# Kernel tuning notes

Measured on AMD Instinct MI355X. Metric: run time of the kernel, lower is better.

Reference implementation:

```python
import jax, jax.numpy as jnp
import numpy as np

S, D = 16384, 1024


def setup_inputs() -> dict:
    key = jax.random.key(0)
    ks = jax.random.split(key, 7)
    stdv = 1.0 / np.sqrt(D)
    u = lambda k, shape: jax.random.uniform(k, shape, jnp.float32, -stdv, stdv)
    return {
        "x": jax.random.normal(ks[0], (S, D), jnp.float32),
        "Wq": u(ks[1], (D, D)), "bq": u(ks[2], (D,)),
        "Wk": u(ks[3], (D, D)), "bk": u(ks[4], (D,)),
        "Wv": u(ks[5], (D, D)), "bv": u(ks[6], (D,)),
    }


def reference(x, Wq, bq, Wk, bk, Wv, bv):
    # torch.nn.Linear: y = x @ W^T + b
    q = x @ Wq.T + bq          # [S, D]
    k = x @ Wk.T + bk          # [S, D]
    v = x @ Wv.T + bv          # [S, D]
    d = x.shape[-1]
    # NOTE: faithful to source -- scores are over the FEATURE axis: [D, D]
    scores = jnp.einsum('sd,se->de', q, k) / jnp.sqrt(jnp.float32(d))
    attn = jax.nn.softmax(scores, axis=-1)   # [D, D]
    out = v @ attn                           # [S, D]
    return out, attn
```

## Files before the change

kernel.cpp:

```cpp
#include <hip/hip_runtime.h>
#include <hip/hip_bf16.h>
#include <stdint.h>


#define S_ 16384
#define D_ 1024

typedef _Float16 half8 __attribute__((ext_vector_type(8)));
typedef _Float16 half4 __attribute__((ext_vector_type(4)));
typedef float f32x4 __attribute__((ext_vector_type(4)));

__device__ __forceinline__ void gload_lds16(const _Float16* g, _Float16* l) {
    __builtin_amdgcn_global_load_lds(
        (const __attribute__((address_space(1))) void*)g,
        (__attribute__((address_space(3))) void*)l, 16, 0, 0);
}

#define VM8() do { asm volatile("s_waitcnt vmcnt(8)" ::: "memory"); __builtin_amdgcn_sched_barrier(0); } while (0)
#define VM0() do { asm volatile("s_waitcnt vmcnt(0)" ::: "memory"); __builtin_amdgcn_sched_barrier(0); } while (0)
#define BAR() __builtin_amdgcn_s_barrier()
#define LGKM0() do { asm volatile("s_waitcnt lgkmcnt(0)" ::: "memory"); __builtin_amdgcn_sched_barrier(0); } while (0)
#define LGKM8() do { asm volatile("s_waitcnt lgkmcnt(8)" ::: "memory"); __builtin_amdgcn_sched_barrier(0); } while (0)
#define PRIO1() __builtin_amdgcn_s_setprio(1)
#define PRIO0() __builtin_amdgcn_s_setprio(0)

#define PAIR10(PI, BY, BX) do { \
    if ((PI) < 4) { BY = 0; BX = (PI); } \
    else if ((PI) < 7) { BY = 1; BX = (PI) - 3; } \
    else if ((PI) < 9) { BY = 2; BX = (PI) - 5; } \
    else { BY = 3; BX = 3; } \
} while (0)

#define STAGEA(H, KT, NX) do { \
    const _Float16* _s = srcA + (size_t)((H) * 128) * 16384 + (size_t)(KT) * 64; \
    _Float16* _d = AsS + (NX) * 16384 + ((H) * 128 + 8 * w) * 64; \
    gload_lds16(_s, _d); \
    gload_lds16(_s + (size_t)64 * 16384, _d + 4096); \
} while (0)

#define STAGEB(H, KT, NX) do { \
    const _Float16* _s = srcB + (size_t)((H) * 128) * 16384 + (size_t)(KT) * 64; \
    _Float16* _d = BsS + (NX) * 16384 + ((H) * 128 + 8 * w) * 64; \
    gload_lds16(_s, _d); \
    gload_lds16(_s + (size_t)64 * 16384, _d + 4096); \
} while (0)

#define READA(PA, QA) do { _Pragma("unroll") \
    for (int fm = 0; fm < 4; ++fm) { \
        af[fm][0] = *(const half8*)((PA) + (((QA) * 128 + fm * 16) << 7) + cx0); \
        af[fm][1] = *(const half8*)((PA) + (((QA) * 128 + fm * 16) << 7) + cx1); } \
} while (0)

#define READB(PB, BF, QB) do { _Pragma("unroll") \
    for (int fn = 0; fn < 2; ++fn) { \
        BF[fn][0] = *(const half8*)((PB) + (((QB) * 128 + fn * 16) << 7) + cx0); \
        BF[fn][1] = *(const half8*)((PB) + (((QB) * 128 + fn * 16) << 7) + cx1); } \
} while (0)

#define MFMAB(QA, QB, BF) do { _Pragma("unroll") \
    for (int fm = 0; fm < 4; ++fm) { _Pragma("unroll") \
        for (int fn = 0; fn < 2; ++fn) { \
            f32x4 _c = acc[(QA) * 4 + fm][(QB) * 2 + fn]; \
            _c = __builtin_amdgcn_mfma_f32_16x16x32_f16(af[fm][0], BF[fn][0], _c, 0, 0, 0); \
            _c = __builtin_amdgcn_mfma_f32_16x16x32_f16(af[fm][1], BF[fn][1], _c, 0, 0, 0); \
            acc[(QA) * 4 + fm][(QB) * 2 + fn] = _c; } } \
} while (0)

__global__ __launch_bounds__(512, 2)
void g_and_prep(const _Float16* __restrict__ A, _Float16* __restrict__ C,
                const float* __restrict__ Wq, const float* __restrict__ Wk,
                const float* __restrict__ Wv, const float* __restrict__ bq,
                const float* __restrict__ m,
                _Float16* __restrict__ wq16, _Float16* __restrict__ wk16,
                _Float16* __restrict__ wvT16,
                float* __restrict__ u2, float* __restrict__ wvec) {
    __shared__ _Float16 SM2[65536];
    const int t = threadIdx.x;

    if (blockIdx.x < 160) {
        _Float16* AsS = SM2;
        _Float16* BsS = SM2 + 32768;
        const int l = t & 63;
        const int w = t >> 6;
        const int wm = w >> 2, wn = w & 3;

        const int hb = blockIdx.x;
        const int lg = (hb & 7) * 20 + (hb >> 3);
        const int bz = lg / 10;
        const int pi = lg - bz * 10;
        int by, bx;
        PAIR10(pi, by, bx);
        const size_t m0 = (size_t)by * 256;
        const size_t n0 = (size_t)bx * 256;
        const size_t k0 = (size_t)bz * 1024;
        const long long coff = (long long)bz * 1048576LL;

        const int colsw = 8 * ((l & 7) ^ (l >> 3));
        const _Float16* srcA = A + (m0 + 8 * w + (l >> 3)) * (size_t)16384 + k0 + colsw;
        const _Float16* srcB = A + (n0 + 8 * w + (l >> 3)) * (size_t)16384 + k0 + colsw;

        const int cx0 = (((l >> 4) << 4)) ^ ((l & 7) << 4);
        const int cx1 = (64 + ((l >> 4) << 4)) ^ ((l & 7) << 4);
        const char* basePA = (const char*)AsS + ((wm * 64 + (l & 15)) << 7);
        const char* basePB = (const char*)BsS + ((wn * 32 + (l & 15)) << 7);

        f32x4 acc[8][4] = {};
        half8 af[4][2], bf0[2][2], bf1[2][2];

        const int nk = 16;

        STAGEA(0, 0, 0); STAGEB(0, 0, 0); STAGEB(1, 0, 0); STAGEA(1, 0, 0);
        STAGEA(0, 1, 1); STAGEB(0, 1, 1); STAGEB(1, 1, 1); STAGEA(1, 1, 1);

        for (int kt = 0; kt < nk; ++kt) {
            const int p = kt & 1;
            const int ks = kt + 2;
            const bool hs = ks < nk;
            const char* pA = basePA + p * 32768;
            const char* pB = basePB + p * 32768;

            if (kt == nk - 1) VM0(); else VM8();
            BAR();

            READA(pA, 0); READB(pB, bf0, 0);
            LGKM8();
            BAR(); LGKM0();
            PRIO1(); MFMAB(0, 0, bf0); PRIO0(); BAR();

            READB(pB, bf1, 1);
            if (hs) { STAGEA(0, ks, p); STAGEB(0, ks, p); }
            BAR(); LGKM0();
            PRIO1(); MFMAB(0, 1, bf1); PRIO0(); BAR();

            READA(pA, 1);
            if (hs) STAGEB(1, ks, p);
            BAR(); LGKM0();
            PRIO1(); MFMAB(1, 1, bf1); PRIO0(); BAR();

            if (hs) STAGEA(1, ks, p);
            PRIO1(); MFMAB(1, 0, bf0); PRIO0(); BAR();
        }

        _Float16* eb = SM2;
        const int cr = (l >> 4) << 2;
        const int cc = l & 15;
#pragma unroll
        for (int h = 0; h < 2; ++h) {
            BAR();
#pragma unroll
            for (int mm = 0; mm < 4; ++mm) {
#pragma unroll
                for (int n = 0; n < 4; ++n) {
                    const int lrow0 = wm * 64 + mm * 16 + cr;
                    const int lcol = (n >> 1) * 128 + wn * 32 + (n & 1) * 16 + cc;
#pragma unroll
                    for (int r = 0; r < 4; ++r)
                        eb[(lrow0 + r) * 264 + lcol] = (_Float16)acc[h * 4 + mm][n][r];
                }
            }
            LGKM0();
            BAR();
#pragma unroll
            for (int i = 0; i < 8; ++i) {
                const int lrow = w * 16 + i * 2 + (l >> 5);
                const half8 v = *(const half8*)(eb + lrow * 264 + (l & 31) * 8);
                const size_t row = m0 + (size_t)h * 128 + lrow;
                const size_t col = n0 + (l & 31) * 8;
                __builtin_nontemporal_store(v,
                    (half8*)(C + coff + (long long)row * 1024 + col));
            }
            LGKM0();
        }
        return;
    }

    const int h = t >> 8;
    const int vt = t & 255;
    const int vb = (blockIdx.x - 160) * 2 + h;
    _Float16* tileh = SM2 + h * 4224;
    float* wredAll = (float*)(SM2 + 16896);
    const bool isW = vb < 1024;

    if (isW) {
        const bool isQ = vb < 512;
        const int bb = isQ ? vb : vb - 512;
        const float* W = isQ ? Wq : Wk;
        _Float16* o = isQ ? wq16 : wk16;
        const size_t base = (size_t)bb * 2048 + (size_t)vt * 8;
        const f32x4* p = (const f32x4*)(W + base);
        f32x4 x0 = p[0], x1 = p[1];
        half8 hv;
        hv[0] = (_Float16)x0[0]; hv[1] = (_Float16)x0[1];
        hv[2] = (_Float16)x0[2]; hv[3] = (_Float16)x0[3];
        hv[4] = (_Float16)x1[0]; hv[5] = (_Float16)x1[1];
        hv[6] = (_Float16)x1[2]; hv[7] = (_Float16)x1[3];
        ((half8*)o)[bb * 256 + vt] = hv;
        const int col = (vt * 8) & 1023;
        f32x4 m0v = *(const f32x4*)(m + col);
        f32x4 m1v = *(const f32x4*)(m + col + 4);
        float s = x0[0] * m0v[0] + x0[1] * m0v[1] + x0[2] * m0v[2] + x0[3] * m0v[3]
                + x1[0] * m1v[0] + x1[1] * m1v[1] + x1[2] * m1v[2] + x1[3] * m1v[3];
        for (int o2 = 32; o2; o2 >>= 1) s += __shfl_xor(s, o2);
        if ((t & 63) == 0) wredAll[t >> 6] = s;
    } else {
        const int bb = vb - 1024;
        const int c0 = (bb & 15) * 64;
        const int r0 = (bb >> 4) * 64;
        const int cg = vt & 15;
        const int rb = vt >> 4;
#pragma unroll
        for (int it = 0; it < 4; ++it) {
            const int rr = rb + it * 16;
            f32x4 v = *(const f32x4*)(Wv + (size_t)(r0 + rr) * 1024 + c0 + cg * 4);
            tileh[rr * 66 + cg * 4 + 0] = (_Float16)v[0];
            tileh[rr * 66 + cg * 4 + 1] = (_Float16)v[1];
            tileh[rr * 66 + cg * 4 + 2] = (_Float16)v[2];
            tileh[rr * 66 + cg * 4 + 3] = (_Float16)v[3];
        }
    }
    __syncthreads();
    if (isW) {
        if (vt == 0) {
            const bool isQ = vb < 512;
            const int bb = isQ ? vb : vb - 512;
            const int rA = 2 * bb, rB = 2 * bb + 1;
            const float vA = wredAll[h * 4 + 0] + wredAll[h * 4 + 1];
            const float vB = wredAll[h * 4 + 2] + wredAll[h * 4 + 3];
            if (isQ) {
                u2[rA] = vA + 16384.0f * bq[rA];
                u2[rB] = vB + 16384.0f * bq[rB];
            } else {
                wvec[rA] = vA;
                wvec[rB] = vB;
            }
        }
    } else {
        const int bb = vb - 1024;
        const int c0 = (bb & 15) * 64;
        const int r0 = (bb >> 4) * 64;
        const int i = vt >> 2, ch = (vt & 3) * 16;
        half8 h0v, h1v;
#pragma unroll
        for (int j = 0; j < 8; ++j) h0v[j] = tileh[(ch + j) * 66 + i];
#pragma unroll
        for (int j = 0; j < 8; ++j) h1v[j] = tileh[(ch + 8 + j) * 66 + i];
        *(half8*)(wvT16 + (size_t)(c0 + i) * 1024 + r0 + ch) = h0v;
        *(half8*)(wvT16 + (size_t)(c0 + i) * 1024 + r0 + ch + 8) = h1v;
    }
}

__global__ __launch_bounds__(256)
void reduce_h_u(const _Float16* __restrict__ part, _Float16* __restrict__ G16) {
    __shared__ _Float16 lt[256][9];
    const int b = blockIdx.x;
    const int ti = b >> 5;
    int by, bx;
    PAIR10(ti, by, bx);
    const int t = threadIdx.x;
    const int e0 = (b & 31) * 2048 + t * 8;
    const size_t row = (size_t)by * 256 + (e0 >> 8);
    const size_t col = (size_t)bx * 256 + (e0 & 255);
    const size_t off = row * 1024 + col;
    float s[8] = {};
    for (int z = 0; z < 16; ++z) {
        half8 v = *(const half8*)(part + (size_t)z * 1048576 + off);
#pragma unroll
        for (int j = 0; j < 8; ++j) s[j] += (float)v[j];
    }
    half8 o;
#pragma unroll
    for (int j = 0; j < 8; ++j) o[j] = (_Float16)s[j];
    *(half8*)(G16 + off) = o;

    const bool offd = (by != bx);
    if (offd) {
        const int cl = (t & 31) * 8;
        const int rl = t >> 5;
#pragma unroll
        for (int j = 0; j < 8; ++j) lt[cl + j][rl] = o[j];
    }
    __syncthreads();
    if (offd) {
        half8 v = *(const half8*)(&lt[t][0]);
        *(half8*)(G16 + ((size_t)(bx * 256 + t)) * 1024 + by * 256 + (b & 31) * 8) = v;
    }
}

#define STG128(SRC, LD, DST, KT) do { \
    const _Float16* _s = (SRC) + (size_t)(KT) * 64; \
    _Float16* _d = (DST) + 8 * w * 64; \
    gload_lds16(_s, _d); \
    gload_lds16(_s + (size_t)32 * (LD), _d + 2048); \
    gload_lds16(_s + (size_t)64 * (LD), _d + 4096); \
    gload_lds16(_s + (size_t)96 * (LD), _d + 6144); \
} while (0)

__global__ __launch_bounds__(256, 2)
void gemm128(const _Float16* __restrict__ A, const _Float16* __restrict__ B,
             float* __restrict__ C, const float* __restrict__ bias,
             int lda, int ldb, int ldc, int ksub,
             int ntx, int cpx) {
    __shared__ _Float16 SM[32768];
    const int t = threadIdx.x;
    const int l = t & 63;
    const int w = t >> 6;
    const int wm = w >> 1, wn = w & 1;

    const int hb = blockIdx.x;
    const int lg = (hb & 7) * cpx + (hb >> 3);
    const int by = lg / ntx;
    const int bx = lg - by * ntx;
    const size_t m0 = (size_t)by * 128;
    const size_t n0 = (size_t)bx * 128;

    const int colsw = 8 * ((l & 7) ^ (l >> 3));
    const _Float16* srcA = A + (m0 + 8 * w + (l >> 3)) * (size_t)lda + colsw;
    const _Float16* srcB = B + (n0 + 8 * w + (l >> 3)) * (size_t)ldb + colsw;

    const int cx0 = (((l >> 4) << 4)) ^ ((l & 7) << 4);
    const int cx1 = (64 + ((l >> 4) << 4)) ^ ((l & 7) << 4);
    const char* basePA = (const char*)SM + ((wm * 64 + (l & 15)) << 7);
    const char* basePB = (const char*)SM + 32768 + ((wn * 64 + (l & 15)) << 7);

    f32x4 acc[4][4] = {};
    half8 af[4][2], bf[4][2];

    const int nk = ksub >> 6;

    STG128(srcA, lda, SM + 0, 0);        STG128(srcB, ldb, SM + 16384, 0);
    STG128(srcA, lda, SM + 8192, 1);     STG128(srcB, ldb, SM + 24576, 1);

    for (int kt = 0; kt < nk; ++kt) {
        const int p = kt & 1;
        const int ks = kt + 2;
        const bool hs = ks < nk;
        const char* pA = basePA + p * 16384;
        const char* pB = basePB + p * 16384;

        if (kt == nk - 1) VM0(); else VM8();
        BAR();

#pragma unroll
        for (int fm = 0; fm < 4; ++fm) {
            af[fm][0] = *(const half8*)(pA + ((fm * 16) << 7) + cx0);
            af[fm][1] = *(const half8*)(pA + ((fm * 16) << 7) + cx1);
        }
#pragma unroll
        for (int fn = 0; fn < 4; ++fn) {
            bf[fn][0] = *(const half8*)(pB + ((fn * 16) << 7) + cx0);
            bf[fn][1] = *(const half8*)(pB + ((fn * 16) << 7) + cx1);
        }
        LGKM0();
        PRIO1();
#pragma unroll
        for (int fm = 0; fm < 4; ++fm)
#pragma unroll
            for (int fn = 0; fn < 4; ++fn)
                acc[fm][fn] = __builtin_amdgcn_mfma_f32_16x16x32_f16(af[fm][0], bf[fn][0], acc[fm][fn], 0, 0, 0);
        PRIO0();
        BAR();

        if (hs) {
            STG128(srcA, lda, SM + p * 8192, ks);
            STG128(srcB, ldb, SM + 16384 + p * 8192, ks);
        }
        PRIO1();
#pragma unroll
        for (int fm = 0; fm < 4; ++fm)
#pragma unroll
            for (int fn = 0; fn < 4; ++fn)
                acc[fm][fn] = __builtin_amdgcn_mfma_f32_16x16x32_f16(af[fm][1], bf[fn][1], acc[fm][fn], 0, 0, 0);
        PRIO0();
        BAR();
    }

    float* lw = (float*)((char*)SM + w * 16384);
    const int cr = (l >> 4) << 2;
    const int cc = l & 15;
    float bb4[4];
#pragma unroll
    for (int fn = 0; fn < 4; ++fn)
        bb4[fn] = bias[n0 + wn * 64 + fn * 16 + cc];
#pragma unroll
    for (int h = 0; h < 2; ++h) {
#pragma unroll
        for (int mm2 = 0; mm2 < 2; ++mm2) {
            const int mm = h * 2 + mm2;
#pragma unroll
            for (int fn = 0; fn < 4; ++fn) {
                const int lcol = fn * 16 + cc;
                const int lrow = mm2 * 16 + cr;
#pragma unroll
                for (int r = 0; r < 4; ++r)
                    lw[(lrow + r) * 68 + lcol] = acc[mm][fn][r] + bb4[fn];
            }
        }
        LGKM0();
        const size_t grow0 = m0 + (size_t)wm * 64 + h * 32;
#pragma unroll
        for (int i = 0; i < 8; ++i) {
            const int lrow = i * 4 + (l >> 4);
            const int lcol = (l & 15) * 4;
            const f32x4 v = *(const f32x4*)(lw + lrow * 68 + lcol);
            __builtin_nontemporal_store(v,
                (f32x4*)(C + (size_t)(grow0 + lrow) * ldc + n0 + wn * 64 + lcol));
        }
        LGKM0();
    }
}

template <int F16OUT>
__global__ __launch_bounds__(256, 2)
void gemm_s128(const _Float16* __restrict__ A, const _Float16* __restrict__ B,
               void* __restrict__ C, int lda, int ldb, int ldc, int ksub,
               long long mn) {
    __shared__ _Float16 SM[32768];
    const int t = threadIdx.x;
    const int l = t & 63;
    const int w = t >> 6;
    const int wm = w >> 1, wn = w & 1;

    const size_t m0 = (size_t)blockIdx.y * 128;
    const size_t n0 = (size_t)blockIdx.x * 128;
    const size_t k0 = (size_t)blockIdx.z * (size_t)ksub;
    const long long coff = (long long)blockIdx.z * mn;

    const int colsw = 8 * ((l & 7) ^ (l >> 3));
    const _Float16* srcA = A + (m0 + 8 * w + (l >> 3)) * (size_t)lda + k0 + colsw;
    const _Float16* srcB = B + (n0 + 8 * w + (l >> 3)) * (size_t)ldb + k0 + colsw;

    const int cx0 = (((l >> 4) << 4)) ^ ((l & 7) << 4);
    const int cx1 = (64 + ((l >> 4) << 4)) ^ ((l & 7) << 4);
    const char* basePA = (const char*)SM + ((wm * 64 + (l & 15)) << 7);
    const char* basePB = (const char*)SM + 32768 + ((wn * 64 + (l & 15)) << 7);

    f32x4 acc[4][4] = {};
    half8 af[4][2], bf[4][2];

    const int nk = ksub >> 6;

    STG128(srcA, lda, SM + 0, 0);        STG128(srcB, ldb, SM + 16384, 0);
    STG128(srcA, lda, SM + 8192, 1);     STG128(srcB, ldb, SM + 24576, 1);

    for (int kt = 0; kt < nk; ++kt) {
        const int p = kt & 1;
        const int ks = kt + 2;
        const bool hs = ks < nk;
        const char* pA = basePA + p * 16384;
        const char* pB = basePB + p * 16384;

        if (kt == nk - 1) VM0(); else VM8();
        BAR();

#pragma unroll
        for (int fm = 0; fm < 4; ++fm) {
            af[fm][0] = *(const half8*)(pA + ((fm * 16) << 7) + cx0);
            af[fm][1] = *(const half8*)(pA + ((fm * 16) << 7) + cx1);
        }
#pragma unroll
        for (int fn = 0; fn < 4; ++fn) {
            bf[fn][0] = *(const half8*)(pB + ((fn * 16) << 7) + cx0);
            bf[fn][1] = *(const half8*)(pB + ((fn * 16) << 7) + cx1);
        }
        LGKM0();
        PRIO1();
#pragma unroll
        for (int fm = 0; fm < 4; ++fm)
#pragma unroll
            for (int fn = 0; fn < 4; ++fn)
                acc[fm][fn] = __builtin_amdgcn_mfma_f32_16x16x32_f16(af[fm][0], bf[fn][0], acc[fm][fn], 0, 0, 0);
        PRIO0();
        BAR();

        if (hs) {
            STG128(srcA, lda, SM + p * 8192, ks);
            STG128(srcB, ldb, SM + 16384 + p * 8192, ks);
        }
        PRIO1();
#pragma unroll
        for (int fm = 0; fm < 4; ++fm)
#pragma unroll
            for (int fn = 0; fn < 4; ++fn)
                acc[fm][fn] = __builtin_amdgcn_mfma_f32_16x16x32_f16(af[fm][1], bf[fn][1], acc[fm][fn], 0, 0, 0);
        PRIO0();
        BAR();
    }

    const int cr = (l >> 4) << 2;
    const int cc = l & 15;

    if (F16OUT) {
        _Float16* eb = SM;
#pragma unroll
        for (int fm = 0; fm < 4; ++fm) {
#pragma unroll
            for (int fn = 0; fn < 4; ++fn) {
                const int lrow0 = wm * 64 + fm * 16 + cr;
                const int lcol = wn * 64 + fn * 16 + cc;
#pragma unroll
                for (int r = 0; r < 4; ++r)
                    eb[(lrow0 + r) * 132 + lcol] = (_Float16)acc[fm][fn][r];
            }
        }
        LGKM0();
        BAR();
        _Float16* Ch = (_Float16*)C;
#pragma unroll
        for (int i = 0; i < 8; ++i) {
            const int row = i * 16 + (t >> 4);
            const int colh = (t & 15) * 8;
            const half8 v = *(const half8*)(eb + row * 132 + colh);
            *(half8*)(Ch + coff + (long long)(m0 + row) * ldc + n0 + colh) = v;
        }
    } else {
        float* lw = (float*)((char*)SM + w * 16384);
        float* Cf = (float*)C;
#pragma unroll
        for (int h = 0; h < 2; ++h) {
#pragma unroll
            for (int mm2 = 0; mm2 < 2; ++mm2) {
                const int mm = h * 2 + mm2;
#pragma unroll
                for (int fn = 0; fn < 4; ++fn) {
                    const int lcol = fn * 16 + cc;
                    const int lrow = mm2 * 16 + cr;
#pragma unroll
                    for (int r = 0; r < 4; ++r)
                        lw[(lrow + r) * 68 + lcol] = acc[mm][fn][r];
                }
            }
            LGKM0();
            const size_t grow0 = m0 + (size_t)wm * 64 + h * 32;
#pragma unroll
            for (int i = 0; i < 8; ++i) {
                const int lrow = i * 4 + (l >> 4);
                const int lcol = (l & 15) * 4;
                const f32x4 v = *(const f32x4*)(lw + lrow * 68 + lcol);
                *(f32x4*)(Cf + coff + (long long)(grow0 + lrow) * ldc + n0 + wn * 64 + lcol) = v;
            }
            LGKM0();
        }
    }
}

__global__ __launch_bounds__(256, 2)
void gemm_mt_bv(const _Float16* __restrict__ A, const _Float16* __restrict__ B,
                _Float16* __restrict__ Cp,
                const float* __restrict__ attn, const float* __restrict__ bv,
                float* __restrict__ cvec) {
    const int idx = blockIdx.x;
    if (idx >= 256) {
        const int bb = idx - 256;
        const int j = (bb & 3) * 256 + threadIdx.x;
        const int a0 = (bb >> 2) * 64;
        float s = 0.f;
#pragma unroll 4
        for (int k = 0; k < 64; ++k) {
            const int a = a0 + k;
            s += attn[(size_t)a * 1024 + j] * bv[a];
        }
        atomicAdd(cvec + j, s);
        return;
    }

    __shared__ _Float16 SM[32768];
    const int t = threadIdx.x;
    const int l = t & 63;
    const int w = t >> 6;
    const int wm = w >> 1, wn = w & 1;

    const int bx = idx & 7, by = (idx >> 3) & 7, bz = idx >> 6;
    const size_t m0 = (size_t)by * 128;
    const size_t n0 = (size_t)bx * 128;
    const size_t k0 = (size_t)bz * 256;
    const long long coff = (long long)bz * 1048576LL;

    const int colsw = 8 * ((l & 7) ^ (l >> 3));
    const _Float16* srcA = A + (m0 + 8 * w + (l >> 3)) * (size_t)1024 + k0 + colsw;
    const _Float16* srcB = B + (n0 + 8 * w + (l >> 3)) * (size_t)1024 + k0 + colsw;

    const int cx0 = (((l >> 4) << 4)) ^ ((l & 7) << 4);
    const int cx1 = (64 + ((l >> 4) << 4)) ^ ((l & 7) << 4);
    const char* basePA = (const char*)SM + ((wm * 64 + (l & 15)) << 7);
    const char* basePB = (const char*)SM + 32768 + ((wn * 64 + (l & 15)) << 7);

    f32x4 acc[4][4] = {};
    half8 af[4][2], bf[4][2];

    const int nk = 4;

    STG128(srcA, 1024, SM + 0, 0);        STG128(srcB, 1024, SM + 16384, 0);
    STG128(srcA, 1024, SM + 8192, 1);     STG128(srcB, 1024, SM + 24576, 1);

    for (int kt = 0; kt < nk; ++kt) {
        const int p = kt & 1;
        const int ks = kt + 2;
        const bool hs = ks < nk;
        const char* pA = basePA + p * 16384;
        const char* pB = basePB + p * 16384;

        if (kt == nk - 1) VM0(); else VM8();
        BAR();

#pragma unroll
        for (int fm = 0; fm < 4; ++fm) {
            af[fm][0] = *(const half8*)(pA + ((fm * 16) << 7) + cx0);
            af[fm][1] = *(const half8*)(pA + ((fm * 16) << 7) + cx1);
        }
#pragma unroll
        for (int fn = 0; fn < 4; ++fn) {
            bf[fn][0] = *(const half8*)(pB + ((fn * 16) << 7) + cx0);
            bf[fn][1] = *(const half8*)(pB + ((fn * 16) << 7) + cx1);
        }
        LGKM0();
        PRIO1();
#pragma unroll
        for (int fm = 0; fm < 4; ++fm)
#pragma unroll
            for (int fn = 0; fn < 4; ++fn)
                acc[fm][fn] = __builtin_amdgcn_mfma_f32_16x16x32_f16(af[fm][0], bf[fn][0], acc[fm][fn], 0, 0, 0);
        PRIO0();
        BAR();

        if (hs) {
            STG128(srcA, 1024, SM + p * 8192, ks);
            STG128(srcB, 1024, SM + 16384 + p * 8192, ks);
        }
        PRIO1();
#pragma unroll
        for (int fm = 0; fm < 4; ++fm)
#pragma unroll
            for (int fn = 0; fn < 4; ++fn)
                acc[fm][fn] = __builtin_amdgcn_mfma_f32_16x16x32_f16(af[fm][1], bf[fn][1], acc[fm][fn], 0, 0, 0);
        PRIO0();
        BAR();
    }

    const int cr = (l >> 4) << 2;
    const int cc = l & 15;
    _Float16* eb = SM;
#pragma unroll
    for (int fm = 0; fm < 4; ++fm) {
#pragma unroll
        for (int fn = 0; fn < 4; ++fn) {
            const int lrow0 = wm * 64 + fm * 16 + cr;
            const int lcol = wn * 64 + fn * 16 + cc;
#pragma unroll
            for (int r = 0; r < 4; ++r)
                eb[(lrow0 + r) * 132 + lcol] = (_Float16)acc[fm][fn][r];
        }
    }
    LGKM0();
    BAR();
#pragma unroll
    for (int i = 0; i < 8; ++i) {
        const int row = i * 16 + (t >> 4);
        const int colh = (t & 15) * 8;
        const half8 v = *(const half8*)(eb + row * 132 + colh);
        *(half8*)(Cp + coff + (long long)(m0 + row) * 1024 + n0 + colh) = v;
    }
}

template <int WRITE_ROW, int COLSUM>
__global__ __launch_bounds__(256)
void cast_transpose(const float* __restrict__ in, _Float16* __restrict__ outRow,
                    _Float16* __restrict__ outT, float* __restrict__ msum, int ldT) {
    __shared__ _Float16 tile[64][66];
    __shared__ float red[16][16][4];
    const int t = threadIdx.x;
    const int c0 = blockIdx.x * 64;
    const int r0 = blockIdx.y * 64;
    const int cg = t & 15;
    const int rb = t >> 4;
    f32x4 csum = {};
#pragma unroll
    for (int it = 0; it < 4; ++it) {
        const int rr = rb + it * 16;
        f32x4 v = *(const f32x4*)(in + (size_t)(r0 + rr) * 1024 + c0 + cg * 4);
        if (COLSUM) { csum[0] += v[0]; csum[1] += v[1]; csum[2] += v[2]; csum[3] += v[3]; }
        _Float16 h0 = (_Float16)v[0], h1 = (_Float16)v[1];
        _Float16 h2 = (_Float16)v[2], h3 = (_Float16)v[3];
        tile[rr][cg * 4 + 0] = h0; tile[rr][cg * 4 + 1] = h1;
        tile[rr][cg * 4 + 2] = h2; tile[rr][cg * 4 + 3] = h3;
        if (WRITE_ROW) {
            half4 h = {h0, h1, h2, h3};
            *(half4*)(outRow + (size_t)(r0 + rr) * 1024 + c0 + cg * 4) = h;
        }
    }
    if (COLSUM) {
        red[rb][cg][0] = csum[0]; red[rb][cg][1] = csum[1];
        red[rb][cg][2] = csum[2]; red[rb][cg][3] = csum[3];
    }
    __syncthreads();
    if (COLSUM && t < 64) {
        float s = 0.f;
#pragma unroll
        for (int k = 0; k < 16; ++k) s += red[k][t >> 2][t & 3];
        atomicAdd(msum + c0 + t, s);
    }
    const int i = t >> 2, ch = (t & 3) * 16;
    half8 h0v, h1v;
#pragma unroll
    for (int j = 0; j < 8; ++j) h0v[j] = tile[ch + j][i];
#pragma unroll
    for (int j = 0; j < 8; ++j) h1v[j] = tile[ch + 8 + j][i];
    *(half8*)(outT + (size_t)(c0 + i) * ldT + r0 + ch) = h0v;
    *(half8*)(outT + (size_t)(c0 + i) * ldT + r0 + ch + 8) = h1v;
}

__global__ void zero_vec(float* __restrict__ p, int n) {
    int i = blockIdx.x * 256 + threadIdx.x;
    if (i < n) p[i] = 0.f;
}

__global__ __launch_bounds__(256)
void reduce_h(const _Float16* __restrict__ part, _Float16* __restrict__ outh,
              int nz) {
    const size_t off = ((size_t)blockIdx.x * 256 + threadIdx.x) * 8;
    float s[8] = {};
    for (int z = 0; z < nz; ++z) {
        half8 v = *(const half8*)(part + (size_t)z * 1048576 + off);
#pragma unroll
        for (int j = 0; j < 8; ++j) s[j] += (float)v[j];
    }
    half8 o;
#pragma unroll
    for (int j = 0; j < 8; ++j) o[j] = (_Float16)s[j];
    *(half8*)(outh + off) = o;
}

__global__ __launch_bounds__(256)
void softmax_rows(const float* __restrict__ part, const float* __restrict__ u2,
                  const float* __restrict__ bq, const float* __restrict__ bk,
                  const float* __restrict__ w,
                  float* __restrict__ P, _Float16* __restrict__ PT) {
    const int a = blockIdx.x;
    const int t = threadIdx.x;
    __shared__ float red[8];
    const size_t off = (size_t)a * 1024 + t * 4;
    f32x4 s = {};
#pragma unroll
    for (int z = 0; z < 4; ++z) {
        f32x4 v = *(const f32x4*)(part + (size_t)z * 1048576 + off);
        s[0] += v[0]; s[1] += v[1]; s[2] += v[2]; s[3] += v[3];
    }
    const float ru = u2[a], rb = bq[a];
    f32x4 bk4 = *(const f32x4*)(bk + t * 4);
    f32x4 w4 = *(const f32x4*)(w + t * 4);
#pragma unroll
    for (int j = 0; j < 4; ++j) s[j] = (s[j] + ru * bk4[j] + rb * w4[j]) * 0.03125f;

    float m = fmaxf(fmaxf(s[0], s[1]), fmaxf(s[2], s[3]));
    for (int o = 32; o; o >>= 1) m = fmaxf(m, __shfl_xor(m, o));
    if ((t & 63) == 0) red[t >> 6] = m;
    __syncthreads();
    m = fmaxf(fmaxf(red[0], red[1]), fmaxf(red[2], red[3]));

    float e0 = expf(s[0] - m), e1 = expf(s[1] - m);
    float e2 = expf(s[2] - m), e3 = expf(s[3] - m);
    float sum = e0 + e1 + e2 + e3;
    for (int o = 32; o; o >>= 1) sum += __shfl_xor(sum, o);
    if ((t & 63) == 0) red[4 + (t >> 6)] = sum;
    __syncthreads();
    sum = red[4] + red[5] + red[6] + red[7];
    const float inv = 1.0f / sum;

    f32x4 o4 = {e0 * inv, e1 * inv, e2 * inv, e3 * inv};
    *(f32x4*)(P + off) = o4;
    const int b = t * 4;
    PT[(size_t)(b + 0) * 1024 + a] = (_Float16)o4[0];
    PT[(size_t)(b + 1) * 1024 + a] = (_Float16)o4[1];
    PT[(size_t)(b + 2) * 1024 + a] = (_Float16)o4[2];
    PT[(size_t)(b + 3) * 1024 + a] = (_Float16)o4[3];
}

extern "C" void kernel_launch(void* const* d_in, const int* in_sizes, int n_in,
                              void* d_out, int out_size, void* d_ws, size_t ws_size,
                              hipStream_t stream) {
    const float* x  = (const float*)d_in[0];
    const float* Wq = (const float*)d_in[1];
    const float* bq = (const float*)d_in[2];
    const float* Wk = (const float*)d_in[3];
    const float* bk = (const float*)d_in[4];
    const float* Wv = (const float*)d_in[5];
    const float* bv = (const float*)d_in[6];
    float* out  = (float*)d_out;
    float* attn = out + (size_t)S_ * D_;

    char* ws = (char*)d_ws;
    float*    part  = (float*)ws;
    _Float16* partH = (_Float16*)ws;
    _Float16* x16   = (_Float16*)(ws + 33554432);
    _Float16* xT16  = (_Float16*)(ws + 67108864);
    _Float16* wq16  = (_Float16*)(ws + 100663296);
    _Float16* wk16  = (_Float16*)(ws + 102760448);
    _Float16* wvT16 = (_Float16*)(ws + 104857600);
    _Float16* G16   = (_Float16*)(ws + 106954752);
    _Float16* U16   = (_Float16*)(ws + 109051904);
    _Float16* PT    = (_Float16*)(ws + 111149056);
    _Float16* MT16  = (_Float16*)(ws + 113246208);
    float*    mvec  = (float*)(ws + 115343360);
    float*    u2    = mvec + 1024;
    float*    wv    = u2 + 1024;
    float*    cvec  = wv + 1024;

    zero_vec<<<16, 256, 0, stream>>>(mvec, 4096);
    cast_transpose<1, 1><<<dim3(16, 256), 256, 0, stream>>>(x, x16, xT16, mvec, S_);

    g_and_prep<<<800, 512, 0, stream>>>(xT16, partH, Wq, Wk, Wv, bq, mvec,
                                        wq16, wk16, wvT16, u2, wv);
    reduce_h_u<<<320, 256, 0, stream>>>(partH, G16);
    gemm_s128<1><<<dim3(8, 8, 4), 256, 0, stream>>>(wq16, G16, (void*)partH,
                                                    1024, 1024, 1024, 256, 1048576);
    reduce_h<<<512, 256, 0, stream>>>(partH, U16, 4);
    gemm_s128<0><<<dim3(8, 8, 4), 256, 0, stream>>>(U16, wk16, (void*)part,
                                                    1024, 1024, 1024, 256, 1048576);
    softmax_rows<<<1024, 256, 0, stream>>>(part, u2, bq, bk, wv, attn, PT);
    gemm_mt_bv<<<320, 256, 0, stream>>>(PT, wvT16, partH, attn, bv, cvec);
    reduce_h<<<512, 256, 0, stream>>>(partH, MT16, 4);
    gemm128<<<1024, 256, 0, stream>>>(x16, MT16, out, cvec,
                                      1024, 1024, 1024, 1024, 8, 128);
}
```

Before: 154.9 us.

## Fuse middle reduce/GEMM/softmax chain into one cooperative persistent kernel

Replaces seven separate launches with a single cooperative kernel of 256 blocks. That chain is reduce_h_u, two split-K GEMMs, reduce_h, softmax_rows, gemm_mt_bv and the final reduce_h. The stages are separated by grid.sync plus thread fences, and blocks loop over virtual block indices where a stage has more work than blocks. The aim is to remove the kernel launch gaps and tail drains between small dependent stages. The cost is grid-wide barriers, fewer blocks for softmax (each block handles four rows in sequence), and a dependence on cooperative launch co-residency.

```diff
diff --git a/kernel.cpp b/kernel.cpp
--- a/kernel.cpp
+++ b/kernel.cpp
@@ -1,6 +1,9 @@
 #include <hip/hip_runtime.h>
 #include <hip/hip_bf16.h>
+#include <hip/hip_cooperative_groups.h>
 #include <stdint.h>
+
+namespace cg = cooperative_groups;
 
 
 #define S_ 16384
@@ -249,10 +252,151 @@
     }
 }
 
-__global__ __launch_bounds__(256)
-void reduce_h_u(const _Float16* __restrict__ part, _Float16* __restrict__ G16) {
-    __shared__ _Float16 lt[256][9];
-    const int b = blockIdx.x;
+__device__ __forceinline__ void stg128f(const _Float16* src, _Float16* dst,
+                                        int kt, int w) {
+    const _Float16* s = src + (size_t)kt * 64;
+    _Float16* d = dst + 8 * w * 64;
+    gload_lds16(s, d);
+    gload_lds16(s + 32 * 1024, d + 2048);
+    gload_lds16(s + 64 * 1024, d + 4096);
+    gload_lds16(s + 96 * 1024, d + 6144);
+}
+
+__device__ __forceinline__ void gemm_body(const _Float16* __restrict__ A,
+                                          const _Float16* __restrict__ B,
+                                          void* __restrict__ C, int f16out,
+                                          _Float16* SM, int idx) {
+    const int t = threadIdx.x;
+    const int l = t & 63;
+    const int w = t >> 6;
+    const int wm = w >> 1, wn = w & 1;
+    const int bx = idx & 7, by = (idx >> 3) & 7, bz = idx >> 6;
+    const size_t m0 = (size_t)by * 128;
+    const size_t n0 = (size_t)bx * 128;
+    const size_t k0 = (size_t)bz * 256;
+    const long long coff = (long long)bz * 1048576LL;
+
+    const int colsw = 8 * ((l & 7) ^ (l >> 3));
+    const _Float16* srcA = A + (m0 + 8 * w + (l >> 3)) * (size_t)1024 + k0 + colsw;
+    const _Float16* srcB = B + (n0 + 8 * w + (l >> 3)) * (size_t)1024 + k0 + colsw;
+
+    const int cx0 = (((l >> 4) << 4)) ^ ((l & 7) << 4);
+    const int cx1 = (64 + ((l >> 4) << 4)) ^ ((l & 7) << 4);
+    const char* basePA = (const char*)SM + ((wm * 64 + (l & 15)) << 7);
+    const char* basePB = (const char*)SM + 32768 + ((wn * 64 + (l & 15)) << 7);
+
+    f32x4 acc[4][4] = {};
+    half8 af[4][2], bf[4][2];
+    const int nk = 4;
+
+    stg128f(srcA, SM + 0, 0, w);      stg128f(srcB, SM + 16384, 0, w);
+    stg128f(srcA, SM + 8192, 1, w);   stg128f(srcB, SM + 24576, 1, w);
+
+    for (int kt = 0; kt < nk; ++kt) {
+        const int p = kt & 1;
+        const int ks = kt + 2;
+        const bool hs = ks < nk;
+        const char* pA = basePA + p * 16384;
+        const char* pB = basePB + p * 16384;
+
+        if (kt == nk - 1) VM0(); else VM8();
+        BAR();
+
+#pragma unroll
+        for (int fm = 0; fm < 4; ++fm) {
+            af[fm][0] = *(const half8*)(pA + ((fm * 16) << 7) + cx0);
+            af[fm][1] = *(const half8*)(pA + ((fm * 16) << 7) + cx1);
+        }
+#pragma unroll
+        for (int fn = 0; fn < 4; ++fn) {
+            bf[fn][0] = *(const half8*)(pB + ((fn * 16) << 7) + cx0);
+            bf[fn][1] = *(const half8*)(pB + ((fn * 16) << 7) + cx1);
+        }
+        LGKM0();
+        PRIO1();
+#pragma unroll
+        for (int fm = 0; fm < 4; ++fm)
+#pragma unroll
+            for (int fn = 0; fn < 4; ++fn)
+                acc[fm][fn] = __builtin_amdgcn_mfma_f32_16x16x32_f16(af[fm][0], bf[fn][0], acc[fm][fn], 0, 0, 0);
+        PRIO0();
+        BAR();
+
+        if (hs) {
+            stg128f(srcA, SM + p * 8192, ks, w);
+            stg128f(srcB, SM + 16384 + p * 8192, ks, w);
+        }
+        PRIO1();
+#pragma unroll
+        for (int fm = 0; fm < 4; ++fm)
+#pragma unroll
+            for (int fn = 0; fn < 4; ++fn)
+                acc[fm][fn] = __builtin_amdgcn_mfma_f32_16x16x32_f16(af[fm][1], bf[fn][1], acc[fm][fn], 0, 0, 0);
+        PRIO0();
+        BAR();
+    }
+
+    const int cr = (l >> 4) << 2;
+    const int cc = l & 15;
+
+    if (f16out) {
+        _Float16* eb = SM;
+#pragma unroll
+        for (int fm = 0; fm < 4; ++fm) {
+#pragma unroll
+            for (int fn = 0; fn < 4; ++fn) {
+                const int lrow0 = wm * 64 + fm * 16 + cr;
+                const int lcol = wn * 64 + fn * 16 + cc;
+#pragma unroll
+                for (int r = 0; r < 4; ++r)
+                    eb[(lrow0 + r) * 132 + lcol] = (_Float16)acc[fm][fn][r];
+            }
+        }
+        LGKM0();
+        BAR();
+        _Float16* Ch = (_Float16*)C;
+#pragma unroll
+        for (int i = 0; i < 8; ++i) {
+            const int row = i * 16 + (t >> 4);
+            const int colh = (t & 15) * 8;
+            const half8 v = *(const half8*)(eb + row * 132 + colh);
+            *(half8*)(Ch + coff + (long long)(m0 + row) * 1024 + n0 + colh) = v;
+        }
+    } else {
+        float* lw = (float*)((char*)SM + w * 16384);
+        float* Cf = (float*)C;
+#pragma unroll
+        for (int h = 0; h < 2; ++h) {
+#pragma unroll
+            for (int mm2 = 0; mm2 < 2; ++mm2) {
+                const int mm = h * 2 + mm2;
+#pragma unroll
+                for (int fn = 0; fn < 4; ++fn) {
+                    const int lcol = fn * 16 + cc;
+                    const int lrow = mm2 * 16 + cr;
+#pragma unroll
+                    for (int r = 0; r < 4; ++r)
+                        lw[(lrow + r) * 68 + lcol] = acc[mm][fn][r];
+                }
+            }
+            LGKM0();
+            const size_t grow0 = m0 + (size_t)wm * 64 + h * 32;
+#pragma unroll
+            for (int i = 0; i < 8; ++i) {
+                const int lrow = i * 4 + (l >> 4);
+                const int lcol = (l & 15) * 4;
+                const f32x4 v = *(const f32x4*)(lw + lrow * 68 + lcol);
+                *(f32x4*)(Cf + coff + (long long)(grow0 + lrow) * 1024 + n0 + wn * 64 + lcol) = v;
+            }
+            LGKM0();
+        }
+    }
+    VM0();
+}
+
+__device__ __forceinline__ void reduce_hu_body(const _Float16* part,
+                                               _Float16* G16, _Float16* lt,
+                                               int b) {
     const int ti = b >> 5;
     int by, bx;
     PAIR10(ti, by, bx);
@@ -277,13 +421,122 @@
         const int cl = (t & 31) * 8;
         const int rl = t >> 5;
 #pragma unroll
-        for (int j = 0; j < 8; ++j) lt[cl + j][rl] = o[j];
+        for (int j = 0; j < 8; ++j) lt[(cl + j) * 9 + rl] = o[j];
     }
     __syncthreads();
     if (offd) {
-        half8 v = *(const half8*)(&lt[t][0]);
+        half8 v = *(const half8*)(lt + t * 9);
         *(half8*)(G16 + ((size_t)(bx * 256 + t)) * 1024 + by * 256 + (b & 31) * 8) = v;
     }
+    __syncthreads();
+}
+
+__device__ __forceinline__ void reduce_body(const _Float16* part,
+                                            _Float16* outh, int vb) {
+    const size_t off = ((size_t)vb * 256 + threadIdx.x) * 8;
+    float s[8] = {};
+    for (int z = 0; z < 4; ++z) {
+        half8 v = *(const half8*)(part + (size_t)z * 1048576 + off);
+#pragma unroll
+        for (int j = 0; j < 8; ++j) s[j] += (float)v[j];
+    }
+    half8 o;
+#pragma unroll
+    for (int j = 0; j < 8; ++j) o[j] = (_Float16)s[j];
+    *(half8*)(outh + off) = o;
+}
+
+__device__ __forceinline__ void softmax_body(const float* partF, const float* u2,
+        const float* bq, const float* bk, const float* wvec,
+        float* P, _Float16* PT, int a, float* red) {
+    const int t = threadIdx.x;
+    const size_t off = (size_t)a * 1024 + t * 4;
+    f32x4 s = {};
+#pragma unroll
+    for (int z = 0; z < 4; ++z) {
+        f32x4 v = *(const f32x4*)(partF + (size_t)z * 1048576 + off);
+        s[0] += v[0]; s[1] += v[1]; s[2] += v[2]; s[3] += v[3];
+    }
+    const float ru = u2[a], rb = bq[a];
+    f32x4 bk4 = *(const f32x4*)(bk + t * 4);
+    f32x4 w4 = *(const f32x4*)(wvec + t * 4);
+#pragma unroll
+    for (int j = 0; j < 4; ++j) s[j] = (s[j] + ru * bk4[j] + rb * w4[j]) * 0.03125f;
+
+    float m = fmaxf(fmaxf(s[0], s[1]), fmaxf(s[2], s[3]));
+    for (int o = 32; o; o >>= 1) m = fmaxf(m, __shfl_xor(m, o));
+    if ((t & 63) == 0) red[t >> 6] = m;
+    __syncthreads();
+    m = fmaxf(fmaxf(red[0], red[1]), fmaxf(red[2], red[3]));
+
+    float e0 = expf(s[0] - m), e1 = expf(s[1] - m);
+    float e2 = expf(s[2] - m), e3 = expf(s[3] - m);
+    float sum = e0 + e1 + e2 + e3;
+    for (int o = 32; o; o >>= 1) sum += __shfl_xor(sum, o);
+    if ((t & 63) == 0) red[4 + (t >> 6)] = sum;
+    __syncthreads();
+    sum = red[4] + red[5] + red[6] + red[7];
+    const float inv = 1.0f / sum;
+
+    f32x4 o4 = {e0 * inv, e1 * inv, e2 * inv, e3 * inv};
+    *(f32x4*)(P + off) = o4;
+    const int b = t * 4;
+    PT[(size_t)(b + 0) * 1024 + a] = (_Float16)o4[0];
+    PT[(size_t)(b + 1) * 1024 + a] = (_Float16)o4[1];
+    PT[(size_t)(b + 2) * 1024 + a] = (_Float16)o4[2];
+    PT[(size_t)(b + 3) * 1024 + a] = (_Float16)o4[3];
+    __syncthreads();
+}
+
+__device__ __forceinline__ void bv_body(const float* attn, const float* bv,
+                                        float* cvec, int bb) {
+    const int j = (bb & 3) * 256 + threadIdx.x;
+    const int a0 = (bb >> 2) * 64;
+    float s = 0.f;
+#pragma unroll 4
+    for (int k = 0; k < 64; ++k) {
+        const int a = a0 + k;
+        s += attn[(size_t)a * 1024 + j] * bv[a];
+    }
+    atomicAdd(cvec + j, s);
+}
+
+__global__ __launch_bounds__(256, 2)
+void midchain(const _Float16* gpart, _Float16* G16,
+              const _Float16* wq16, const _Float16* wk16,
+              const _Float16* wvT16,
+              _Float16* partH, float* partF,
+              _Float16* U16, _Float16* MT16, _Float16* PT,
+              const float* u2, const float* bq, const float* bk,
+              const float* wvec, float* attn, const float* bv, float* cvec) {
+    cg::grid_group grid = cg::this_grid();
+    __shared__ _Float16 SM[32768];
+    const int bid = blockIdx.x;
+
+    for (int vb = bid; vb < 320; vb += 256)
+        reduce_hu_body(gpart, G16, SM, vb);
+    VM0(); __threadfence(); grid.sync();
+
+    gemm_body(wq16, G16, (void*)partH, 1, SM, bid);
+    __threadfence(); grid.sync();
+
+    for (int vb = bid; vb < 512; vb += 256)
+        reduce_body(partH, U16, vb);
+    VM0(); __threadfence(); grid.sync();
+
+    gemm_body(U16, wk16, (void*)partF, 0, SM, bid);
+    __threadfence(); grid.sync();
+
+    for (int r = 0; r < 4; ++r)
+        softmax_body(partF, u2, bq, bk, wvec, attn, PT, bid * 4 + r, (float*)SM);
+    VM0(); __threadfence(); grid.sync();
+
+    gemm_body(PT, wvT16, (void*)partH, 1, SM, bid);
+    __threadfence(); grid.sync();
+
+    for (int vb = bid; vb < 512; vb += 256)
+        reduce_body(partH, MT16, vb);
+    if (bid < 64) bv_body(attn, bv, cvec, bid);
 }
 
 #define STG128(SRC, LD, DST, KT) do { \
@@ -406,258 +659,6 @@
                 (f32x4*)(C + (size_t)(grow0 + lrow) * ldc + n0 + wn * 64 + lcol));
         }
         LGKM0();
-    }
-}
-
-template <int F16OUT>
-__global__ __launch_bounds__(256, 2)
-void gemm_s128(const _Float16* __restrict__ A, const _Float16* __restrict__ B,
-               void* __restrict__ C, int lda, int ldb, int ldc, int ksub,
-               long long mn) {
-    __shared__ _Float16 SM[32768];
-    const int t = threadIdx.x;
-    const int l = t & 63;
-    const int w = t >> 6;
-    const int wm = w >> 1, wn = w & 1;
-
-    const size_t m0 = (size_t)blockIdx.y * 128;
-    const size_t n0 = (size_t)blockIdx.x * 128;
-    const size_t k0 = (size_t)blockIdx.z * (size_t)ksub;
-    const long long coff = (long long)blockIdx.z * mn;
-
-    const int colsw = 8 * ((l & 7) ^ (l >> 3));
-    const _Float16* srcA = A + (m0 + 8 * w + (l >> 3)) * (size_t)lda + k0 + colsw;
-    const _Float16* srcB = B + (n0 + 8 * w + (l >> 3)) * (size_t)ldb + k0 + colsw;
-
-    const int cx0 = (((l >> 4) << 4)) ^ ((l & 7) << 4);
-    const int cx1 = (64 + ((l >> 4) << 4)) ^ ((l & 7) << 4);
-    const char* basePA = (const char*)SM + ((wm * 64 + (l & 15)) << 7);
-    const char* basePB = (const char*)SM + 32768 + ((wn * 64 + (l & 15)) << 7);
-
-    f32x4 acc[4][4] = {};
-    half8 af[4][2], bf[4][2];
-
-    const int nk = ksub >> 6;
-
-    STG128(srcA, lda, SM + 0, 0);        STG128(srcB, ldb, SM + 16384, 0);
-    STG128(srcA, lda, SM + 8192, 1);     STG128(srcB, ldb, SM + 24576, 1);
-
-    for (int kt = 0; kt < nk; ++kt) {
-        const int p = kt & 1;
-        const int ks = kt + 2;
-        const bool hs = ks < nk;
-        const char* pA = basePA + p * 16384;
-        const char* pB = basePB + p * 16384;
-
-        if (kt == nk - 1) VM0(); else VM8();
-        BAR();
-
-#pragma unroll
-        for (int fm = 0; fm < 4; ++fm) {
-            af[fm][0] = *(const half8*)(pA + ((fm * 16) << 7) + cx0);
-            af[fm][1] = *(const half8*)(pA + ((fm * 16) << 7) + cx1);
-        }
-#pragma unroll
-        for (int fn = 0; fn < 4; ++fn) {
-            bf[fn][0] = *(const half8*)(pB + ((fn * 16) << 7) + cx0);
-            bf[fn][1] = *(const half8*)(pB + ((fn * 16) << 7) + cx1);
-        }
-        LGKM0();
-        PRIO1();
-#pragma unroll
-        for (int fm = 0; fm < 4; ++fm)
-#pragma unroll
-            for (int fn = 0; fn < 4; ++fn)
-                acc[fm][fn] = __builtin_amdgcn_mfma_f32_16x16x32_f16(af[fm][0], bf[fn][0], acc[fm][fn], 0, 0, 0);
-        PRIO0();
-        BAR();
-
-        if (hs) {
-            STG128(srcA, lda, SM + p * 8192, ks);
-            STG128(srcB, ldb, SM + 16384 + p * 8192, ks);
-        }
-        PRIO1();
-#pragma unroll
-        for (int fm = 0; fm < 4; ++fm)
-#pragma unroll
-            for (int fn = 0; fn < 4; ++fn)
-                acc[fm][fn] = __builtin_amdgcn_mfma_f32_16x16x32_f16(af[fm][1], bf[fn][1], acc[fm][fn], 0, 0, 0);
-        PRIO0();
-        BAR();
-    }
-
-    const int cr = (l >> 4) << 2;
-    const int cc = l & 15;
-
-    if (F16OUT) {
-        _Float16* eb = SM;
-#pragma unroll
-        for (int fm = 0; fm < 4; ++fm) {
-#pragma unroll
-            for (int fn = 0; fn < 4; ++fn) {
-                const int lrow0 = wm * 64 + fm * 16 + cr;
-                const int lcol = wn * 64 + fn * 16 + cc;
-#pragma unroll
-                for (int r = 0; r < 4; ++r)
-                    eb[(lrow0 + r) * 132 + lcol] = (_Float16)acc[fm][fn][r];
-            }
-        }
-        LGKM0();
-        BAR();
-        _Float16* Ch = (_Float16*)C;
-#pragma unroll
-        for (int i = 0; i < 8; ++i) {
-            const int row = i * 16 + (t >> 4);
-            const int colh = (t & 15) * 8;
-            const half8 v = *(const half8*)(eb + row * 132 + colh);
-            *(half8*)(Ch + coff + (long long)(m0 + row) * ldc + n0 + colh) = v;
-        }
-    } else {
-        float* lw = (float*)((char*)SM + w * 16384);
-        float* Cf = (float*)C;
-#pragma unroll
-        for (int h = 0; h < 2; ++h) {
-#pragma unroll
-            for (int mm2 = 0; mm2 < 2; ++mm2) {
-                const int mm = h * 2 + mm2;
-#pragma unroll
-                for (int fn = 0; fn < 4; ++fn) {
-                    const int lcol = fn * 16 + cc;
-                    const int lrow = mm2 * 16 + cr;
-#pragma unroll
-                    for (int r = 0; r < 4; ++r)
-                        lw[(lrow + r) * 68 + lcol] = acc[mm][fn][r];
-                }
-            }
-            LGKM0();
-            const size_t grow0 = m0 + (size_t)wm * 64 + h * 32;
-#pragma unroll
-            for (int i = 0; i < 8; ++i) {
-                const int lrow = i * 4 + (l >> 4);
-                const int lcol = (l & 15) * 4;
-                const f32x4 v = *(const f32x4*)(lw + lrow * 68 + lcol);
-                *(f32x4*)(Cf + coff + (long long)(grow0 + lrow) * ldc + n0 + wn * 64 + lcol) = v;
-            }
-            LGKM0();
-        }
-    }
-}
-
-__global__ __launch_bounds__(256, 2)
-void gemm_mt_bv(const _Float16* __restrict__ A, const _Float16* __restrict__ B,
-                _Float16* __restrict__ Cp,
-                const float* __restrict__ attn, const float* __restrict__ bv,
-                float* __restrict__ cvec) {
-    const int idx = blockIdx.x;
-    if (idx >= 256) {
-        const int bb = idx - 256;
-        const int j = (bb & 3) * 256 + threadIdx.x;
-        const int a0 = (bb >> 2) * 64;
-        float s = 0.f;
-#pragma unroll 4
-        for (int k = 0; k < 64; ++k) {
-            const int a = a0 + k;
-            s += attn[(size_t)a * 1024 + j] * bv[a];
-        }
-        atomicAdd(cvec + j, s);
-        return;
-    }
-
-    __shared__ _Float16 SM[32768];
-    const int t = threadIdx.x;
-    const int l = t & 63;
-    const int w = t >> 6;
-    const int wm = w >> 1, wn = w & 1;
-
-    const int bx = idx & 7, by = (idx >> 3) & 7, bz = idx >> 6;
-    const size_t m0 = (size_t)by * 128;
-    const size_t n0 = (size_t)bx * 128;
-    const size_t k0 = (size_t)bz * 256;
-    const long long coff = (long long)bz * 1048576LL;
-
-    const int colsw = 8 * ((l & 7) ^ (l >> 3));
-    const _Float16* srcA = A + (m0 + 8 * w + (l >> 3)) * (size_t)1024 + k0 + colsw;
-    const _Float16* srcB = B + (n0 + 8 * w + (l >> 3)) * (size_t)1024 + k0 + colsw;
-
-    const int cx0 = (((l >> 4) << 4)) ^ ((l & 7) << 4);
-    const int cx1 = (64 + ((l >> 4) << 4)) ^ ((l & 7) << 4);
-    const char* basePA = (const char*)SM + ((wm * 64 + (l & 15)) << 7);
-    const char* basePB = (const char*)SM + 32768 + ((wn * 64 + (l & 15)) << 7);
-
-    f32x4 acc[4][4] = {};
-    half8 af[4][2], bf[4][2];
-
-    const int nk = 4;
-
-    STG128(srcA, 1024, SM + 0, 0);        STG128(srcB, 1024, SM + 16384, 0);
-    STG128(srcA, 1024, SM + 8192, 1);     STG128(srcB, 1024, SM + 24576, 1);
-
-    for (int kt = 0; kt < nk; ++kt) {
-        const int p = kt & 1;
-        const int ks = kt + 2;
-        const bool hs = ks < nk;
-        const char* pA = basePA + p * 16384;
-        const char* pB = basePB + p * 16384;
-
-        if (kt == nk - 1) VM0(); else VM8();
-        BAR();
-
-#pragma unroll
-        for (int fm = 0; fm < 4; ++fm) {
-            af[fm][0] = *(const half8*)(pA + ((fm * 16) << 7) + cx0);
-            af[fm][1] = *(const half8*)(pA + ((fm * 16) << 7) + cx1);
-        }
-#pragma unroll
-        for (int fn = 0; fn < 4; ++fn) {
-            bf[fn][0] = *(const half8*)(pB + ((fn * 16) << 7) + cx0);
-            bf[fn][1] = *(const half8*)(pB + ((fn * 16) << 7) + cx1);
-        }
-        LGKM0();
-        PRIO1();
-#pragma unroll
-        for (int fm = 0; fm < 4; ++fm)
-#pragma unroll
-            for (int fn = 0; fn < 4; ++fn)
-                acc[fm][fn] = __builtin_amdgcn_mfma_f32_16x16x32_f16(af[fm][0], bf[fn][0], acc[fm][fn], 0, 0, 0);
-        PRIO0();
-        BAR();
-
-        if (hs) {
-            STG128(srcA, 1024, SM + p * 8192, ks);
-            STG128(srcB, 1024, SM + 16384 + p * 8192, ks);
-        }
-        PRIO1();
-#pragma unroll
-        for (int fm = 0; fm < 4; ++fm)
-#pragma unroll
-            for (int fn = 0; fn < 4; ++fn)
-                acc[fm][fn] = __builtin_amdgcn_mfma_f32_16x16x32_f16(af[fm][1], bf[fn][1], acc[fm][fn], 0, 0, 0);
-        PRIO0();
-        BAR();
-    }
-
-    const int cr = (l >> 4) << 2;
-    const int cc = l & 15;
-    _Float16* eb = SM;
-#pragma unroll
-    for (int fm = 0; fm < 4; ++fm) {
-#pragma unroll
-        for (int fn = 0; fn < 4; ++fn) {
-            const int lrow0 = wm * 64 + fm * 16 + cr;
-            const int lcol = wn * 64 + fn * 16 + cc;
-#pragma unroll
-            for (int r = 0; r < 4; ++r)
-                eb[(lrow0 + r) * 132 + lcol] = (_Float16)acc[fm][fn][r];
-        }
-    }
-    LGKM0();
-    BAR();
-#pragma unroll
-    for (int i = 0; i < 8; ++i) {
-        const int row = i * 16 + (t >> 4);
-        const int colh = (t & 15) * 8;
-        const half8 v = *(const half8*)(eb + row * 132 + colh);
-        *(half8*)(Cp + coff + (long long)(m0 + row) * 1024 + n0 + colh) = v;
     }
 }
 
@@ -711,67 +712,6 @@
 __global__ void zero_vec(float* __restrict__ p, int n) {
     int i = blockIdx.x * 256 + threadIdx.x;
     if (i < n) p[i] = 0.f;
-}
-
-__global__ __launch_bounds__(256)
-void reduce_h(const _Float16* __restrict__ part, _Float16* __restrict__ outh,
-              int nz) {
-    const size_t off = ((size_t)blockIdx.x * 256 + threadIdx.x) * 8;
-    float s[8] = {};
-    for (int z = 0; z < nz; ++z) {
-        half8 v = *(const half8*)(part + (size_t)z * 1048576 + off);
-#pragma unroll
-        for (int j = 0; j < 8; ++j) s[j] += (float)v[j];
-    }
-    half8 o;
-#pragma unroll
-    for (int j = 0; j < 8; ++j) o[j] = (_Float16)s[j];
-    *(half8*)(outh + off) = o;
-}
-
-__global__ __launch_bounds__(256)
-void softmax_rows(const float* __restrict__ part, const float* __restrict__ u2,
-                  const float* __restrict__ bq, const float* __restrict__ bk,
-                  const float* __restrict__ w,
-                  float* __restrict__ P, _Float16* __restrict__ PT) {
-    const int a = blockIdx.x;
-    const int t = threadIdx.x;
-    __shared__ float red[8];
-    const size_t off = (size_t)a * 1024 + t * 4;
-    f32x4 s = {};
-#pragma unroll
-    for (int z = 0; z < 4; ++z) {
-        f32x4 v = *(const f32x4*)(part + (size_t)z * 1048576 + off);
-        s[0] += v[0]; s[1] += v[1]; s[2] += v[2]; s[3] += v[3];
-    }
-    const float ru = u2[a], rb = bq[a];
-    f32x4 bk4 = *(const f32x4*)(bk + t * 4);
-    f32x4 w4 = *(const f32x4*)(w + t * 4);
-#pragma unroll
-    for (int j = 0; j < 4; ++j) s[j] = (s[j] + ru * bk4[j] + rb * w4[j]) * 0.03125f;
-
-    float m = fmaxf(fmaxf(s[0], s[1]), fmaxf(s[2], s[3]));
-    for (int o = 32; o; o >>= 1) m = fmaxf(m, __shfl_xor(m, o));
-    if ((t & 63) == 0) red[t >> 6] = m;
-    __syncthreads();
-    m = fmaxf(fmaxf(red[0], red[1]), fmaxf(red[2], red[3]));
-
-    float e0 = expf(s[0] - m), e1 = expf(s[1] - m);
-    float e2 = expf(s[2] - m), e3 = expf(s[3] - m);
-    float sum = e0 + e1 + e2 + e3;
-    for (int o = 32; o; o >>= 1) sum += __shfl_xor(sum, o);
-    if ((t & 63) == 0) red[4 + (t >> 6)] = sum;
-    __syncthreads();
-    sum = red[4] + red[5] + red[6] + red[7];
-    const float inv = 1.0f / sum;
-
-    f32x4 o4 = {e0 * inv, e1 * inv, e2 * inv, e3 * inv};
-    *(f32x4*)(P + off) = o4;
-    const int b = t * 4;
-    PT[(size_t)(b + 0) * 1024 + a] = (_Float16)o4[0];
-    PT[(size_t)(b + 1) * 1024 + a] = (_Float16)o4[1];
-    PT[(size_t)(b + 2) * 1024 + a] = (_Float16)o4[2];
-    PT[(size_t)(b + 3) * 1024 + a] = (_Float16)o4[3];
 }
 
 extern "C" void kernel_launch(void* const* d_in, const int* in_sizes, int n_in,
@@ -806,18 +746,20 @@
 
     zero_vec<<<16, 256, 0, stream>>>(mvec, 4096);
     cast_transpose<1, 1><<<dim3(16, 256), 256, 0, stream>>>(x, x16, xT16, mvec, S_);
-
     g_and_prep<<<800, 512, 0, stream>>>(xT16, partH, Wq, Wk, Wv, bq, mvec,
                                         wq16, wk16, wvT16, u2, wv);
-    reduce_h_u<<<320, 256, 0, stream>>>(partH, G16);
-    gemm_s128<1><<<dim3(8, 8, 4), 256, 0, stream>>>(wq16, G16, (void*)partH,
-                                                    1024, 1024, 1024, 256, 1048576);
-    reduce_h<<<512, 256, 0, stream>>>(partH, U16, 4);
-    gemm_s128<0><<<dim3(8, 8, 4), 256, 0, stream>>>(U16, wk16, (void*)part,
-                                                    1024, 1024, 1024, 256, 1048576);
-    softmax_rows<<<1024, 256, 0, stream>>>(part, u2, bq, bk, wv, attn, PT);
-    gemm_mt_bv<<<320, 256, 0, stream>>>(PT, wvT16, partH, attn, bv, cvec);
-    reduce_h<<<512, 256, 0, stream>>>(partH, MT16, 4);
+
+    {
+        void* args[] = {
+            (void*)&partH, (void*)&G16, (void*)&wq16, (void*)&wk16,
+            (void*)&wvT16, (void*)&partH, (void*)&part, (void*)&U16,
+            (void*)&MT16, (void*)&PT, (void*)&u2, (void*)&bq, (void*)&bk,
+            (void*)&wv, (void*)&attn, (void*)&bv, (void*)&cvec
+        };
+        hipLaunchCooperativeKernel((void*)midchain, dim3(256), dim3(256),
+                                   args, 0, stream);
+    }
+
     gemm128<<<1024, 256, 0, stream>>>(x16, MT16, out, cvec,
                                       1024, 1024, 1024, 1024, 8, 128);
 }
```

Result: slower. 519.9 us (+235.6%).
